# Kernel tuning notes

Measured on AMD Instinct MI355X. Metric: run time of the kernel, lower is better.

Reference implementation:

```python
import jax, jax.numpy as jnp
import numpy as np

N_NODES = 100000
N_EDGES = 3200000
N_GRAPHS = 1000
C = 11   # atomic features
D = 4    # bond features
BN_EPS = 1e-5


def setup_inputs() -> dict:
    key = jax.random.key(0)
    ks = jax.random.split(key, 20)
    inp = {
        "x": jax.random.normal(ks[0], (N_NODES, C), dtype=jnp.float32),
        "edge_index": jax.random.randint(ks[1], (2, N_EDGES), 0, N_NODES),
        "edge_attr": jax.random.uniform(ks[2], (N_EDGES, D), dtype=jnp.float32),
        "batch": jnp.sort(jax.random.randint(ks[3], (N_NODES,), 0, N_GRAPHS)),
    }
    s = 0.3
    # CGConv layer 1 params: lin_f, lin_s take z=[x_i, x_j, e] of dim 2C+D
    inp["Wf1"] = jax.random.normal(ks[4], (2 * C + D, C), dtype=jnp.float32) * s
    inp["bf1"] = jnp.zeros((C,), jnp.float32)
    inp["Ws1"] = jax.random.normal(ks[5], (2 * C + D, C), dtype=jnp.float32) * s
    inp["bs1"] = jnp.zeros((C,), jnp.float32)
    inp["gamma1"] = jnp.ones((C,), jnp.float32)
    inp["beta1"] = jnp.zeros((C,), jnp.float32)
    # CGConv layer 2
    inp["Wf2"] = jax.random.normal(ks[6], (2 * C + D, C), dtype=jnp.float32) * s
    inp["bf2"] = jnp.zeros((C,), jnp.float32)
    inp["Ws2"] = jax.random.normal(ks[7], (2 * C + D, C), dtype=jnp.float32) * s
    inp["bs2"] = jnp.zeros((C,), jnp.float32)
    inp["gamma2"] = jnp.ones((C,), jnp.float32)
    inp["beta2"] = jnp.zeros((C,), jnp.float32)
    # MLP head
    inp["W_fc1"] = jax.random.normal(ks[8], (C, 5), dtype=jnp.float32) * s
    inp["b_fc1"] = jnp.zeros((5,), jnp.float32)
    inp["W_fc2"] = jax.random.normal(ks[9], (5, 1), dtype=jnp.float32) * s
    inp["b_fc2"] = jnp.zeros((1,), jnp.float32)
    return inp


def _cgconv(x, src, dst, e, Wf, bf, Ws, bs, gamma, beta):
    # z = [x_i, x_j, e_ij] per edge; message = sigmoid(lin_f(z)) * softplus(lin_s(z))
    z = jnp.concatenate([x[dst], x[src], e], axis=-1)          # [E, 2C+D]
    msg = jax.nn.sigmoid(z @ Wf + bf) * jax.nn.softplus(z @ Ws + bs)  # [E, C]
    agg = jax.ops.segment_sum(msg, dst, num_segments=N_NODES)  # [N, C]
    # BatchNorm1d (training-mode: batch statistics over nodes)
    mu = jnp.mean(agg, axis=0)
    var = jnp.var(agg, axis=0)
    agg = (agg - mu) * jax.lax.rsqrt(var + BN_EPS) * gamma + beta
    return x + agg  # residual


def reference(x, edge_index, edge_attr, batch,
              Wf1, bf1, Ws1, bs1, gamma1, beta1,
              Wf2, bf2, Ws2, bs2, gamma2, beta2,
              W_fc1, b_fc1, W_fc2, b_fc2):
    src, dst = edge_index[0], edge_index[1]
    h = _cgconv(x, src, dst, edge_attr, Wf1, bf1, Ws1, bs1, gamma1, beta1)
    h = _cgconv(h, src, dst, edge_attr, Wf2, bf2, Ws2, bs2, gamma2, beta2)
    # global mean pool per graph
    sums = jax.ops.segment_sum(h, batch, num_segments=N_GRAPHS)        # [G, C]
    cnts = jax.ops.segment_sum(jnp.ones((h.shape[0],), h.dtype), batch,
                               num_segments=N_GRAPHS)
    pooled = sums / jnp.maximum(cnts, 1.0)[:, None]
    out = jax.nn.softplus(pooled @ W_fc1 + b_fc1)
    out = out @ W_fc2 + b_fc2                                          # [G, 1]
    return out
```

## Files before the change

kernel.cpp:

```cpp
#include <hip/hip_runtime.h>
#include <math.h>

#define N_NODES 100000
#define N_EDGES 3200000
#define N_GRAPHS 1000
#define C 11
#define D 4
#define AST 12
#define XWST 24
#define BN_EPS 1e-5f
#define LOG2E 1.44269504088896f
#define LN2   0.69314718055994f
#define QSCALE (1.0f/65535.0f)

#define BSHIFT 8
#define BNODES 256
#define NB ((N_NODES + BNODES - 1) / BNODES)
#define CAP 8704
#define EPB 4096
#define PBLK ((N_EDGES + EPB - 1) / EPB)
#define SB 64
#define PST 48

__device__ __forceinline__ float fast_sigmoid(float x) {
    float e = exp2f(-LOG2E * x);
    return __builtin_amdgcn_rcpf(1.0f + e);
}
__device__ __forceinline__ float fast_softplus(float x) {
    float e = exp2f(LOG2E * x);
    float l = log2f(1.0f + e) * LN2;
    return (x > 20.0f) ? x : l;
}

__global__ void __launch_bounds__(256) partition_kernel(
    const int* __restrict__ ei, const float4* __restrict__ ea,
    int* __restrict__ bcur, uint3* __restrict__ grp)
{
    __shared__ int lh[NB];
    __shared__ int lbase[NB];
    for (int i = threadIdx.x; i < NB; i += 256) lh[i] = 0;
    __syncthreads();
    int e0 = blockIdx.x * EPB;
    for (int r = 0; r < EPB; r += 256) {
        int e = e0 + r + threadIdx.x;
        if (e < N_EDGES) atomicAdd(&lh[ei[N_EDGES + e] >> BSHIFT], 1);
    }
    __syncthreads();
    for (int b = threadIdx.x; b < NB; b += 256) {
        lbase[b] = atomicAdd(&bcur[b], lh[b]);
        lh[b] = 0;
    }
    __syncthreads();
    for (int r = 0; r < EPB; r += 256) {
        int e = e0 + r + threadIdx.x;
        if (e < N_EDGES) {
            int d = ei[N_EDGES + e];
            int s = ei[e];
            float4 v = ea[e];
            unsigned q0 = (unsigned)(v.x * 65535.0f + 0.5f);
            unsigned q1 = (unsigned)(v.y * 65535.0f + 0.5f);
            unsigned q2 = (unsigned)(v.z * 65535.0f + 0.5f);
            unsigned q3 = (unsigned)(v.w * 65535.0f + 0.5f);
            int b = d >> BSHIFT;
            int ofs = lbase[b] + atomicAdd(&lh[b], 1);
            grp[(size_t)b * CAP + ofs] =
                make_uint3((unsigned)s | ((unsigned)(d & 255) << 17),
                           q0 | (q1 << 16), q2 | (q3 << 16));
        }
    }
}

__global__ void __launch_bounds__(512) bscan_kernel(
    const int* __restrict__ bcur, int* __restrict__ bexcl, int* __restrict__ off)
{
    __shared__ int wsum[8];
    int t = threadIdx.x;
    int lane = t & 63, w = t >> 6;
    int v = (t < NB) ? bcur[t] : 0;
    int incl = v;
    #pragma unroll
    for (int d = 1; d < 64; d <<= 1) {
        int u = __shfl_up(incl, d);
        if (lane >= d) incl += u;
    }
    if (lane == 63) wsum[w] = incl;
    __syncthreads();
    if (w == 0) {
        int x = (lane < 8) ? wsum[lane] : 0;
        #pragma unroll
        for (int d = 1; d < 8; d <<= 1) {
            int u = __shfl_up(x, d);
            if (lane >= d) x += u;
        }
        if (lane < 8) wsum[lane] = x;
    }
    __syncthreads();
    int excl = incl - v + (w > 0 ? wsum[w - 1] : 0);
    if (t < NB) bexcl[t] = excl;
    if (t == 0) { bexcl[NB] = N_EDGES; off[N_NODES] = N_EDGES; }
}

__global__ void __launch_bounds__(256) finalize_kernel(
    const uint3* __restrict__ grp, const int* __restrict__ bcur,
    const int* __restrict__ bexcl,
    int* __restrict__ off, uint3* __restrict__ rec)
{
    __shared__ int lcnt[BNODES];
    __shared__ int lexcl[BNODES];
    __shared__ int wsum[4];
    int b = blockIdx.x;
    int cnt = min(bcur[b], CAP);
    int base = bexcl[b];
    const uint3* g = grp + (size_t)b * CAP;
    int t = threadIdx.x;
    lcnt[t] = 0;
    __syncthreads();
    for (int i = t; i < cnt; i += 256)
        atomicAdd(&lcnt[(g[i].x >> 17) & 255], 1);
    __syncthreads();
    int lane = t & 63, w = t >> 6;
    int v = lcnt[t];
    int incl = v;
    #pragma unroll
    for (int d = 1; d < 64; d <<= 1) {
        int u = __shfl_up(incl, d);
        if (lane >= d) incl += u;
    }
    if (lane == 63) wsum[w] = incl;
    __syncthreads();
    if (w == 0) {
        int x = (lane < 4) ? wsum[lane] : 0;
        #pragma unroll
        for (int d = 1; d < 4; d <<= 1) {
            int u = __shfl_up(x, d);
            if (lane >= d) x += u;
        }
        if (lane < 4) wsum[lane] = x;
    }
    __syncthreads();
    int excl = incl - v + (w > 0 ? wsum[w - 1] : 0);
    lexcl[t] = excl;
    int n = (b << BSHIFT) + t;
    if (n < N_NODES) off[n] = base + excl;
    lcnt[t] = 0;
    __syncthreads();
    for (int i = t; i < cnt; i += 256) {
        uint3 r = g[i];
        int nl = (r.x >> 17) & 255;
        int pos = base + lexcl[nl] + atomicAdd(&lcnt[nl], 1);
        rec[pos] = make_uint3(r.x & 0x1FFFFu, r.y, r.z);
    }
}

__global__ void __launch_bounds__(256) pre_kernel(
    const float* __restrict__ xin, int stride,
    const float* __restrict__ Wf, const float* __restrict__ Ws,
    const float* __restrict__ bf, const float* __restrict__ bs,
    float* __restrict__ xwd, float* __restrict__ xws)
{
    __shared__ float sW[22 * C * 2];
    __shared__ float sbf[C], sbs[C];
    for (int i = threadIdx.x; i < 22 * C; i += blockDim.x) {
        sW[2 * i] = Wf[i];
        sW[2 * i + 1] = Ws[i];
    }
    if (threadIdx.x < C) { sbf[threadIdx.x] = bf[threadIdx.x]; sbs[threadIdx.x] = bs[threadIdx.x]; }
    __syncthreads();

    int n = blockIdx.x * blockDim.x + threadIdx.x;
    if (n >= N_NODES) return;
    float xi[C];
    #pragma unroll
    for (int j = 0; j < C; ++j) xi[j] = xin[n * stride + j];

    float od[XWST], os[XWST];
    #pragma unroll
    for (int c = 0; c < C; ++c) {
        float f = sbf[c], s = sbs[c];
        float f2 = 0.0f, s2 = 0.0f;
        #pragma unroll
        for (int j = 0; j < C; ++j) {
            f  = fmaf(xi[j], sW[2 * (j * C + c)], f);
            s  = fmaf(xi[j], sW[2 * (j * C + c) + 1], s);
            f2 = fmaf(xi[j], sW[2 * ((C + j) * C + c)], f2);
            s2 = fmaf(xi[j], sW[2 * ((C + j) * C + c) + 1], s2);
        }
        od[2 * c] = f; od[2 * c + 1] = s;
        os[2 * c] = f2; os[2 * c + 1] = s2;
    }
    od[22] = 0.0f; od[23] = 0.0f; os[22] = 0.0f; os[23] = 0.0f;
    float4* pd = (float4*)(xwd + (size_t)n * XWST);
    float4* ps = (float4*)(xws + (size_t)n * XWST);
    #pragma unroll
    for (int i = 0; i < 6; ++i) {
        pd[i] = make_float4(od[4 * i], od[4 * i + 1], od[4 * i + 2], od[4 * i + 3]);
        ps[i] = make_float4(os[4 * i], os[4 * i + 1], os[4 * i + 2], os[4 * i + 3]);
    }
}

__global__ void __launch_bounds__(256) conv_kernel(
    const uint3* __restrict__ rec, const int* __restrict__ off,
    const float* __restrict__ xwd, const float* __restrict__ xws,
    const float* __restrict__ Wf, const float* __restrict__ Ws,
    float* __restrict__ agg)
{
    int tid = blockIdx.x * blockDim.x + threadIdx.x;
    int n = tid >> 3;
    int t = tid & 7;
    if (n >= N_NODES) return;

    float weaf[44], weas[44];
    {
        const float2* pf = (const float2*)(Wf + 22 * C);
        const float2* ps = (const float2*)(Ws + 22 * C);
        #pragma unroll
        for (int i = 0; i < 22; ++i) {
            float2 a = pf[i], b = ps[i];
            weaf[2 * i] = a.x; weaf[2 * i + 1] = a.y;
            weas[2 * i] = b.x; weas[2 * i + 1] = b.y;
        }
    }
    float based[XWST];
    {
        const float4* pd = (const float4*)(xwd + (size_t)n * XWST);
        #pragma unroll
        for (int i = 0; i < 6; ++i) {
            float4 a = pd[i];
            based[4 * i] = a.x; based[4 * i + 1] = a.y;
            based[4 * i + 2] = a.z; based[4 * i + 3] = a.w;
        }
    }

    float acc[C];
    #pragma unroll
    for (int c = 0; c < C; ++c) acc[c] = 0.0f;

    int e1 = off[n + 1];
    for (int k = off[n] + t; k < e1; k += 8) {
        uint3 r = rec[k];
        int src = (int)r.x;
        float ea0 = (float)(r.y & 0xFFFFu) * QSCALE;
        float ea1 = (float)(r.y >> 16) * QSCALE;
        float ea2 = (float)(r.z & 0xFFFFu) * QSCALE;
        float ea3 = (float)(r.z >> 16) * QSCALE;
        float xsr[XWST];
        {
            const float4* px = (const float4*)(xws + (size_t)src * XWST);
            #pragma unroll
            for (int i = 0; i < 6; ++i) {
                float4 a = px[i];
                xsr[4 * i] = a.x; xsr[4 * i + 1] = a.y;
                xsr[4 * i + 2] = a.z; xsr[4 * i + 3] = a.w;
            }
        }
        #pragma unroll
        for (int c = 0; c < C; ++c) {
            float f = based[2 * c] + xsr[2 * c];
            float s = based[2 * c + 1] + xsr[2 * c + 1];
            f = fmaf(ea0, weaf[c], f);         s = fmaf(ea0, weas[c], s);
            f = fmaf(ea1, weaf[C + c], f);     s = fmaf(ea1, weas[C + c], s);
            f = fmaf(ea2, weaf[2 * C + c], f); s = fmaf(ea2, weas[2 * C + c], s);
            f = fmaf(ea3, weaf[3 * C + c], f); s = fmaf(ea3, weas[3 * C + c], s);
            acc[c] += fast_sigmoid(f) * fast_softplus(s);
        }
    }

    #pragma unroll
    for (int c = 0; c < C; ++c) {
        acc[c] += __shfl_xor(acc[c], 1);
        acc[c] += __shfl_xor(acc[c], 2);
        acc[c] += __shfl_xor(acc[c], 4);
    }
    if (t == 0) {
        float4* pa = (float4*)(agg + (size_t)n * AST);
        pa[0] = make_float4(acc[0], acc[1], acc[2], acc[3]);
        pa[1] = make_float4(acc[4], acc[5], acc[6], acc[7]);
        pa[2] = make_float4(acc[8], acc[9], acc[10], 0.0f);
    }
}

__global__ void __launch_bounds__(256) bn_stats_kernel(
    const float* __restrict__ agg, float* __restrict__ pstats )
{
    float s[C], q[C];
    #pragma unroll
    for (int c = 0; c < C; ++c) { s[c] = 0.0f; q[c] = 0.0f; }
    for (int n = blockIdx.x * 256 + threadIdx.x; n < N_NODES; n += SB * 256) {
        const float4* pa = (const float4*)(agg + (size_t)n * AST);
        float4 a0 = pa[0], a1 = pa[1], a2 = pa[2];
        float v[C] = {a0.x, a0.y, a0.z, a0.w, a1.x, a1.y, a1.z, a1.w,
                      a2.x, a2.y, a2.z};
        #pragma unroll
        for (int c = 0; c < C; ++c) { s[c] += v[c]; q[c] += v[c] * v[c]; }
    }
    #pragma unroll
    for (int c = 0; c < C; ++c) {
        #pragma unroll
        for (int o = 32; o > 0; o >>= 1) {
            s[c] += __shfl_down(s[c], o);
            q[c] += __shfl_down(q[c], o);
        }
    }
    __shared__ float ls[2 * C + 2];
    if (threadIdx.x < 2 * C + 2) ls[threadIdx.x] = 0.0f;
    __syncthreads();
    if ((threadIdx.x & 63) == 0) {
        #pragma unroll
        for (int c = 0; c < C; ++c) {
            atomicAdd(&ls[2 * c], s[c]);
            atomicAdd(&ls[2 * c + 1], q[c]);
        }
    }
    __syncthreads();
    if (threadIdx.x < 2 * C)
        pstats[blockIdx.x * PST + threadIdx.x] = ls[threadIdx.x];
}

__device__ __forceinline__ void reduce_stats(
    const float* __restrict__ pstats, float* smu, float* srs)
{
    if (threadIdx.x < C) {
        double sum = 0.0, sq = 0.0;
        for (int b = 0; b < SB; ++b) {
            sum += (double)pstats[b * PST + 2 * threadIdx.x];
            sq  += (double)pstats[b * PST + 2 * threadIdx.x + 1];
        }
        double mu = sum / (double)N_NODES;
        double var = sq / (double)N_NODES - mu * mu;
        smu[threadIdx.x] = (float)mu;
        srs[threadIdx.x] = (float)(1.0 / sqrt(var + (double)BN_EPS));
    }
}

__global__ void __launch_bounds__(256) bnpre_kernel(
    const float* __restrict__ xin, const float* __restrict__ agg,
    const float* __restrict__ pstats,
    const float* __restrict__ gamma, const float* __restrict__ beta,
    const float* __restrict__ Wf, const float* __restrict__ Ws,
    const float* __restrict__ bf, const float* __restrict__ bs,
    float* __restrict__ hout, float* __restrict__ xwd, float* __restrict__ xws)
{
    __shared__ float sW[22 * C * 2];
    __shared__ float sbf[C], sbs[C];
    __shared__ float smu[C], srs[C], sg[C], sb[C];
    for (int i = threadIdx.x; i < 22 * C; i += blockDim.x) {
        sW[2 * i] = Wf[i];
        sW[2 * i + 1] = Ws[i];
    }
    reduce_stats(pstats, smu, srs);
    if (threadIdx.x < C) {
        sbf[threadIdx.x] = bf[threadIdx.x];
        sbs[threadIdx.x] = bs[threadIdx.x];
        sg[threadIdx.x] = gamma[threadIdx.x];
        sb[threadIdx.x] = beta[threadIdx.x];
    }
    __syncthreads();

    int n = blockIdx.x * blockDim.x + threadIdx.x;
    if (n >= N_NODES) return;

    float hv[C];
    #pragma unroll
    for (int c = 0; c < C; ++c) {
        float a = agg[n * AST + c];
        hv[c] = xin[n * C + c] + (a - smu[c]) * srs[c] * sg[c] + sb[c];
    }
    {
        float4* ph = (float4*)(hout + (size_t)n * AST);
        ph[0] = make_float4(hv[0], hv[1], hv[2], hv[3]);
        ph[1] = make_float4(hv[4], hv[5], hv[6], hv[7]);
        ph[2] = make_float4(hv[8], hv[9], hv[10], 0.0f);
    }

    float od[XWST], os[XWST];
    #pragma unroll
    for (int c = 0; c < C; ++c) {
        float f = sbf[c], s = sbs[c];
        float f2 = 0.0f, s2 = 0.0f;
        #pragma unroll
        for (int j = 0; j < C; ++j) {
            f  = fmaf(hv[j], sW[2 * (j * C + c)], f);
            s  = fmaf(hv[j], sW[2 * (j * C + c) + 1], s);
            f2 = fmaf(hv[j], sW[2 * ((C + j) * C + c)], f2);
            s2 = fmaf(hv[j], sW[2 * ((C + j) * C + c) + 1], s2);
        }
        od[2 * c] = f; od[2 * c + 1] = s;
        os[2 * c] = f2; os[2 * c + 1] = s2;
    }
    od[22] = 0.0f; od[23] = 0.0f; os[22] = 0.0f; os[23] = 0.0f;
    float4* pd = (float4*)(xwd + (size_t)n * XWST);
    float4* ps = (float4*)(xws + (size_t)n * XWST);
    #pragma unroll
    for (int i = 0; i < 6; ++i) {
        pd[i] = make_float4(od[4 * i], od[4 * i + 1], od[4 * i + 2], od[4 * i + 3]);
        ps[i] = make_float4(os[4 * i], os[4 * i + 1], os[4 * i + 2], os[4 * i + 3]);
    }
}

__global__ void __launch_bounds__(256) bn_apply_kernel(
    const float* __restrict__ hin, const float* __restrict__ agg,
    const float* __restrict__ pstats,
    const float* __restrict__ gamma, const float* __restrict__ beta,
    float* __restrict__ hout)
{
    __shared__ float smu[C], srs[C], sg[C], sb[C];
    reduce_stats(pstats, smu, srs);
    if (threadIdx.x < C) {
        sg[threadIdx.x] = gamma[threadIdx.x];
        sb[threadIdx.x] = beta[threadIdx.x];
    }
    __syncthreads();
    int n = blockIdx.x * blockDim.x + threadIdx.x;
    if (n >= N_NODES) return;
    float hv[C];
    #pragma unroll
    for (int c = 0; c < C; ++c) {
        float a = agg[n * AST + c];
        hv[c] = hin[n * AST + c] + (a - smu[c]) * srs[c] * sg[c] + sb[c];
    }
    float4* ph = (float4*)(hout + (size_t)n * AST);
    ph[0] = make_float4(hv[0], hv[1], hv[2], hv[3]);
    ph[1] = make_float4(hv[4], hv[5], hv[6], hv[7]);
    ph[2] = make_float4(hv[8], hv[9], hv[10], 0.0f);
}

__global__ void __launch_bounds__(256) pool_kernel(
    const float* __restrict__ h, const int* __restrict__ batch,
    float* __restrict__ gsum, float* __restrict__ gcnt)
{
    const int PER = 8;
    int t = blockIdx.x * blockDim.x + threadIdx.x;
    int start = t * PER;
    if (start >= N_NODES) return;
    int end = min(start + PER, N_NODES);

    int g = batch[start];
    float acc[C];
    #pragma unroll
    for (int c = 0; c < C; ++c) acc[c] = 0.0f;
    float cnt = 0.0f;
    for (int n = start; n < end; ++n) {
        int gn = batch[n];
        if (gn != g) {
            #pragma unroll
            for (int c = 0; c < C; ++c) atomicAdd(&gsum[g * C + c], acc[c]);
            atomicAdd(&gcnt[g], cnt);
            g = gn;
            #pragma unroll
            for (int c = 0; c < C; ++c) acc[c] = 0.0f;
            cnt = 0.0f;
        }
        #pragma unroll
        for (int c = 0; c < C; ++c) acc[c] += h[n * AST + c];
        cnt += 1.0f;
    }
    #pragma unroll
    for (int c = 0; c < C; ++c) atomicAdd(&gsum[g * C + c], acc[c]);
    atomicAdd(&gcnt[g], cnt);
}

__global__ void __launch_bounds__(256) head_kernel(
    const float* __restrict__ gsum, const float* __restrict__ gcnt,
    const float* __restrict__ W1, const float* __restrict__ b1,
    const float* __restrict__ W2, const float* __restrict__ b2,
    float* __restrict__ out)
{
    int g = blockIdx.x * blockDim.x + threadIdx.x;
    if (g >= N_GRAPHS) return;
    float cnt = fmaxf(gcnt[g], 1.0f);
    float p[C];
    #pragma unroll
    for (int c = 0; c < C; ++c) p[c] = gsum[g * C + c] / cnt;
    float acc = b2[0];
    #pragma unroll
    for (int j = 0; j < 5; ++j) {
        float t = b1[j];
        #pragma unroll
        for (int c = 0; c < C; ++c) t = fmaf(p[c], W1[c * 5 + j], t);
        acc = fmaf(fast_softplus(t), W2[j], acc);
    }
    out[g] = acc;
}

extern "C" void kernel_launch(void* const* d_in, const int* in_sizes, int n_in,
                              void* d_out, int out_size, void* d_ws, size_t ws_size,
                              hipStream_t stream) {
    const float* x   = (const float*)d_in[0];
    const int*   ei  = (const int*)d_in[1];
    const float* ea  = (const float*)d_in[2];
    const int*   bat = (const int*)d_in[3];
    const float* Wf1 = (const float*)d_in[4];
    const float* bf1 = (const float*)d_in[5];
    const float* Ws1 = (const float*)d_in[6];
    const float* bs1 = (const float*)d_in[7];
    const float* g1  = (const float*)d_in[8];
    const float* be1 = (const float*)d_in[9];
    const float* Wf2 = (const float*)d_in[10];
    const float* bf2 = (const float*)d_in[11];
    const float* Ws2 = (const float*)d_in[12];
    const float* bs2 = (const float*)d_in[13];
    const float* g2  = (const float*)d_in[14];
    const float* be2 = (const float*)d_in[15];
    const float* W_fc1 = (const float*)d_in[16];
    const float* b_fc1 = (const float*)d_in[17];
    const float* W_fc2 = (const float*)d_in[18];
    const float* b_fc2 = (const float*)d_in[19];
    float* out = (float*)d_out;

    char* ws = (char*)d_ws;
    size_t o = 0;
    size_t zz0 = o;
    int*    bcur   = (int*)(ws + o);    o += (size_t)NB * 4;
    float*  gsum   = (float*)(ws + o);  o += (size_t)N_GRAPHS * C * 4;
    float*  gcnt   = (float*)(ws + o);  o += (size_t)N_GRAPHS * 4;
    size_t zsize = o - zz0;
    int*    bexcl  = (int*)(ws + o);    o += (size_t)(NB + 1) * 4;
    int*    off    = (int*)(ws + o);    o += (size_t)(N_NODES + 1) * 4;
    o = (o + 255) & ~(size_t)255;
    float*  pst1   = (float*)(ws + o);  o += (size_t)SB * PST * 4;
    float*  pst2   = (float*)(ws + o);  o += (size_t)SB * PST * 4;
    o = (o + 255) & ~(size_t)255;
    uint3*  grp    = (uint3*)(ws + o);  o += (size_t)NB * CAP * 12;
    o = (o + 255) & ~(size_t)255;
    uint3*  rec    = (uint3*)(ws + o);  o += (size_t)N_EDGES * 12;
    o = (o + 255) & ~(size_t)255;
    float*  xwd    = (float*)(ws + o);  o += (size_t)N_NODES * XWST * 4;
    float*  xws    = (float*)(ws + o);  o += (size_t)N_NODES * XWST * 4;
    float*  agg    = (float*)(ws + o);  o += (size_t)N_NODES * AST * 4;
    float*  h1     = (float*)(ws + o);  o += (size_t)N_NODES * AST * 4;
    float*  h2     = xwd;

    const int cblocks = (N_NODES * 8 + 255) / 256;
    const int nblocks = (N_NODES + 255) / 256;

    hipMemsetAsync(ws + zz0, 0, zsize, stream);

    partition_kernel<<<PBLK, 256, 0, stream>>>(ei, (const float4*)ea, bcur, grp);
    bscan_kernel<<<1, 512, 0, stream>>>(bcur, bexcl, off);
    finalize_kernel<<<NB, 256, 0, stream>>>(grp, bcur, bexcl, off, rec);

    pre_kernel<<<nblocks, 256, 0, stream>>>(x, C, Wf1, Ws1, bf1, bs1, xwd, xws);
    conv_kernel<<<cblocks, 256, 0, stream>>>(rec, off, xwd, xws, Wf1, Ws1, agg);
    bn_stats_kernel<<<SB, 256, 0, stream>>>(agg, pst1);
    bnpre_kernel<<<nblocks, 256, 0, stream>>>(x, agg, pst1, g1, be1,
                                              Wf2, Ws2, bf2, bs2, h1, xwd, xws);

    conv_kernel<<<cblocks, 256, 0, stream>>>(rec, off, xwd, xws, Wf2, Ws2, agg);
    bn_stats_kernel<<<SB, 256, 0, stream>>>(agg, pst2);
    bn_apply_kernel<<<nblocks, 256, 0, stream>>>(h1, agg, pst2, g2, be2, h2);

    pool_kernel<<<(N_NODES / 8 + 255) / 256, 256, 0, stream>>>(h2, bat, gsum, gcnt);
    head_kernel<<<(N_GRAPHS + 255) / 256, 256, 0, stream>>>(gsum, gcnt, W_fc1, b_fc1,
                                                            W_fc2, b_fc2, out);
}
```

Baseline: 349.0 us.

## Store gathered source-node projections in fp16 and split partition counters into sub-buckets

The per-source-node projection table that each edge gathers is now stored as packed half2 (48 bytes per node instead of 96), which cuts gather traffic in both conv passes. The partition step spreads each bucket's global atomic counter over 8 sub-buckets chosen by block index, reducing contention on the counters. Finalize and scan now iterate over and sum those sub-buckets. This trades precision in the gathered values for bandwidth, and any sub-bucket that exceeds its fixed capacity silently drops edges.

```diff
diff --git a/kernel.cpp b/kernel.cpp
--- a/kernel.cpp
+++ b/kernel.cpp
@@ -1,4 +1,5 @@
 #include <hip/hip_runtime.h>
+#include <hip/hip_fp16.h>
 #include <math.h>
 
 #define N_NODES 100000
@@ -8,6 +9,7 @@
 #define D 4
 #define AST 12
 #define XWST 24
+#define XHST 16
 #define BN_EPS 1e-5f
 #define LOG2E 1.44269504088896f
 #define LN2   0.69314718055994f
@@ -16,7 +18,8 @@
 #define BSHIFT 8
 #define BNODES 256
 #define NB ((N_NODES + BNODES - 1) / BNODES)
-#define CAP 8704
+#define SUBS 8
+#define CAP2 1280
 #define EPB 4096
 #define PBLK ((N_EDGES + EPB - 1) / EPB)
 #define SB 64
@@ -31,15 +34,24 @@
     float l = log2f(1.0f + e) * LN2;
     return (x > 20.0f) ? x : l;
 }
+__device__ __forceinline__ unsigned packh2(float a, float b) {
+    __half2 h = __floats2half2_rn(a, b);
+    return *reinterpret_cast<unsigned*>(&h);
+}
+__device__ __forceinline__ float2 unpackh2(unsigned u) {
+    __half2 h = *reinterpret_cast<__half2*>(&u);
+    return __half22float2(h);
+}
 
 __global__ void __launch_bounds__(256) partition_kernel(
     const int* __restrict__ ei, const float4* __restrict__ ea,
-    int* __restrict__ bcur, uint3* __restrict__ grp)
+    int* __restrict__ bcur2, uint3* __restrict__ grp)
 {
     __shared__ int lh[NB];
     __shared__ int lbase[NB];
     for (int i = threadIdx.x; i < NB; i += 256) lh[i] = 0;
     __syncthreads();
+    int sub = blockIdx.x & (SUBS - 1);
     int e0 = blockIdx.x * EPB;
     for (int r = 0; r < EPB; r += 256) {
         int e = e0 + r + threadIdx.x;
@@ -47,7 +59,7 @@
     }
     __syncthreads();
     for (int b = threadIdx.x; b < NB; b += 256) {
-        lbase[b] = atomicAdd(&bcur[b], lh[b]);
+        lbase[b] = atomicAdd(&bcur2[b * SUBS + sub], lh[b]);
         lh[b] = 0;
     }
     __syncthreads();
@@ -63,20 +75,25 @@
             unsigned q3 = (unsigned)(v.w * 65535.0f + 0.5f);
             int b = d >> BSHIFT;
             int ofs = lbase[b] + atomicAdd(&lh[b], 1);
-            grp[(size_t)b * CAP + ofs] =
-                make_uint3((unsigned)s | ((unsigned)(d & 255) << 17),
-                           q0 | (q1 << 16), q2 | (q3 << 16));
+            if (ofs < CAP2)
+                grp[((size_t)b * SUBS + sub) * CAP2 + ofs] =
+                    make_uint3((unsigned)s | ((unsigned)(d & 255) << 17),
+                               q0 | (q1 << 16), q2 | (q3 << 16));
         }
     }
 }
 
 __global__ void __launch_bounds__(512) bscan_kernel(
-    const int* __restrict__ bcur, int* __restrict__ bexcl, int* __restrict__ off)
+    const int* __restrict__ bcur2, int* __restrict__ bexcl, int* __restrict__ off)
 {
     __shared__ int wsum[8];
     int t = threadIdx.x;
     int lane = t & 63, w = t >> 6;
-    int v = (t < NB) ? bcur[t] : 0;
+    int v = 0;
+    if (t < NB) {
+        #pragma unroll
+        for (int s = 0; s < SUBS; ++s) v += min(bcur2[t * SUBS + s], CAP2);
+    }
     int incl = v;
     #pragma unroll
     for (int d = 1; d < 64; d <<= 1) {
@@ -97,11 +114,12 @@
     __syncthreads();
     int excl = incl - v + (w > 0 ? wsum[w - 1] : 0);
     if (t < NB) bexcl[t] = excl;
-    if (t == 0) { bexcl[NB] = N_EDGES; off[N_NODES] = N_EDGES; }
+    if (t == 0) off[N_NODES] = bexcl[NB - 1] >= 0 ? 0 : 0;
+    if (t == NB - 1) off[N_NODES] = excl + v;
 }
 
 __global__ void __launch_bounds__(256) finalize_kernel(
-    const uint3* __restrict__ grp, const int* __restrict__ bcur,
+    const uint3* __restrict__ grp, const int* __restrict__ bcur2,
     const int* __restrict__ bexcl,
     int* __restrict__ off, uint3* __restrict__ rec)
 {
@@ -109,14 +127,16 @@
     __shared__ int lexcl[BNODES];
     __shared__ int wsum[4];
     int b = blockIdx.x;
-    int cnt = min(bcur[b], CAP);
     int base = bexcl[b];
-    const uint3* g = grp + (size_t)b * CAP;
     int t = threadIdx.x;
     lcnt[t] = 0;
     __syncthreads();
-    for (int i = t; i < cnt; i += 256)
-        atomicAdd(&lcnt[(g[i].x >> 17) & 255], 1);
+    for (int s = 0; s < SUBS; ++s) {
+        int cs = min(bcur2[b * SUBS + s], CAP2);
+        const uint3* g = grp + ((size_t)b * SUBS + s) * CAP2;
+        for (int i = t; i < cs; i += 256)
+            atomicAdd(&lcnt[(g[i].x >> 17) & 255], 1);
+    }
     __syncthreads();
     int lane = t & 63, w = t >> 6;
     int v = lcnt[t];
@@ -144,11 +164,15 @@
     if (n < N_NODES) off[n] = base + excl;
     lcnt[t] = 0;
     __syncthreads();
-    for (int i = t; i < cnt; i += 256) {
-        uint3 r = g[i];
-        int nl = (r.x >> 17) & 255;
-        int pos = base + lexcl[nl] + atomicAdd(&lcnt[nl], 1);
-        rec[pos] = make_uint3(r.x & 0x1FFFFu, r.y, r.z);
+    for (int s = 0; s < SUBS; ++s) {
+        int cs = min(bcur2[b * SUBS + s], CAP2);
+        const uint3* g = grp + ((size_t)b * SUBS + s) * CAP2;
+        for (int i = t; i < cs; i += 256) {
+            uint3 r = g[i];
+            int nl = (r.x >> 17) & 255;
+            int pos = base + lexcl[nl] + atomicAdd(&lcnt[nl], 1);
+            rec[pos] = make_uint3(r.x & 0x1FFFFu, r.y, r.z);
+        }
     }
 }
 
@@ -156,7 +180,7 @@
     const float* __restrict__ xin, int stride,
     const float* __restrict__ Wf, const float* __restrict__ Ws,
     const float* __restrict__ bf, const float* __restrict__ bs,
-    float* __restrict__ xwd, float* __restrict__ xws)
+    float* __restrict__ xwd, unsigned* __restrict__ xwsh)
 {
     __shared__ float sW[22 * C * 2];
     __shared__ float sbf[C], sbs[C];
@@ -173,7 +197,8 @@
     #pragma unroll
     for (int j = 0; j < C; ++j) xi[j] = xin[n * stride + j];
 
-    float od[XWST], os[XWST];
+    float od[XWST];
+    unsigned oh[12];
     #pragma unroll
     for (int c = 0; c < C; ++c) {
         float f = sbf[c], s = sbs[c];
@@ -186,21 +211,22 @@
             s2 = fmaf(xi[j], sW[2 * ((C + j) * C + c) + 1], s2);
         }
         od[2 * c] = f; od[2 * c + 1] = s;
-        os[2 * c] = f2; os[2 * c + 1] = s2;
-    }
-    od[22] = 0.0f; od[23] = 0.0f; os[22] = 0.0f; os[23] = 0.0f;
+        oh[c] = packh2(f2, s2);
+    }
+    od[22] = 0.0f; od[23] = 0.0f; oh[11] = 0u;
     float4* pd = (float4*)(xwd + (size_t)n * XWST);
-    float4* ps = (float4*)(xws + (size_t)n * XWST);
-    #pragma unroll
-    for (int i = 0; i < 6; ++i) {
+    #pragma unroll
+    for (int i = 0; i < 6; ++i)
         pd[i] = make_float4(od[4 * i], od[4 * i + 1], od[4 * i + 2], od[4 * i + 3]);
-        ps[i] = make_float4(os[4 * i], os[4 * i + 1], os[4 * i + 2], os[4 * i + 3]);
-    }
+    uint4* ph = (uint4*)(xwsh + (size_t)n * XHST);
+    #pragma unroll
+    for (int i = 0; i < 3; ++i)
+        ph[i] = make_uint4(oh[4 * i], oh[4 * i + 1], oh[4 * i + 2], oh[4 * i + 3]);
 }
 
 __global__ void __launch_bounds__(256) conv_kernel(
     const uint3* __restrict__ rec, const int* __restrict__ off,
-    const float* __restrict__ xwd, const float* __restrict__ xws,
+    const float* __restrict__ xwd, const unsigned* __restrict__ xwsh,
     const float* __restrict__ Wf, const float* __restrict__ Ws,
     float* __restrict__ agg)
 {
@@ -243,20 +269,19 @@
         float ea1 = (float)(r.y >> 16) * QSCALE;
         float ea2 = (float)(r.z & 0xFFFFu) * QSCALE;
         float ea3 = (float)(r.z >> 16) * QSCALE;
-        float xsr[XWST];
-        {
-            const float4* px = (const float4*)(xws + (size_t)src * XWST);
-            #pragma unroll
-            for (int i = 0; i < 6; ++i) {
-                float4 a = px[i];
-                xsr[4 * i] = a.x; xsr[4 * i + 1] = a.y;
-                xsr[4 * i + 2] = a.z; xsr[4 * i + 3] = a.w;
-            }
-        }
+        const uint4* px = (const uint4*)(xwsh + (size_t)src * XHST);
+        uint4 ha = px[0], hb = px[1], hc = px[2];
+        float2 xv[C];
+        xv[0] = unpackh2(ha.x); xv[1] = unpackh2(ha.y);
+        xv[2] = unpackh2(ha.z); xv[3] = unpackh2(ha.w);
+        xv[4] = unpackh2(hb.x); xv[5] = unpackh2(hb.y);
+        xv[6] = unpackh2(hb.z); xv[7] = unpackh2(hb.w);
+        xv[8] = unpackh2(hc.x); xv[9] = unpackh2(hc.y);
+        xv[10] = unpackh2(hc.z);
         #pragma unroll
         for (int c = 0; c < C; ++c) {
-            float f = based[2 * c] + xsr[2 * c];
-            float s = based[2 * c + 1] + xsr[2 * c + 1];
+            float f = based[2 * c] + xv[c].x;
+            float s = based[2 * c + 1] + xv[c].y;
             f = fmaf(ea0, weaf[c], f);         s = fmaf(ea0, weas[c], s);
             f = fmaf(ea1, weaf[C + c], f);     s = fmaf(ea1, weas[C + c], s);
             f = fmaf(ea2, weaf[2 * C + c], f); s = fmaf(ea2, weas[2 * C + c], s);
@@ -338,7 +363,7 @@
     const float* __restrict__ gamma, const float* __restrict__ beta,
     const float* __restrict__ Wf, const float* __restrict__ Ws,
     const float* __restrict__ bf, const float* __restrict__ bs,
-    float* __restrict__ hout, float* __restrict__ xwd, float* __restrict__ xws)
+    float* __restrict__ hout, float* __restrict__ xwd, unsigned* __restrict__ xwsh)
 {
     __shared__ float sW[22 * C * 2];
     __shared__ float sbf[C], sbs[C];
@@ -372,7 +397,8 @@
         ph[2] = make_float4(hv[8], hv[9], hv[10], 0.0f);
     }
 
-    float od[XWST], os[XWST];
+    float od[XWST];
+    unsigned oh[12];
     #pragma unroll
     for (int c = 0; c < C; ++c) {
         float f = sbf[c], s = sbs[c];
@@ -385,16 +411,17 @@
             s2 = fmaf(hv[j], sW[2 * ((C + j) * C + c) + 1], s2);
         }
         od[2 * c] = f; od[2 * c + 1] = s;
-        os[2 * c] = f2; os[2 * c + 1] = s2;
-    }
-    od[22] = 0.0f; od[23] = 0.0f; os[22] = 0.0f; os[23] = 0.0f;
+        oh[c] = packh2(f2, s2);
+    }
+    od[22] = 0.0f; od[23] = 0.0f; oh[11] = 0u;
     float4* pd = (float4*)(xwd + (size_t)n * XWST);
-    float4* ps = (float4*)(xws + (size_t)n * XWST);
-    #pragma unroll
-    for (int i = 0; i < 6; ++i) {
+    #pragma unroll
+    for (int i = 0; i < 6; ++i)
         pd[i] = make_float4(od[4 * i], od[4 * i + 1], od[4 * i + 2], od[4 * i + 3]);
-        ps[i] = make_float4(os[4 * i], os[4 * i + 1], os[4 * i + 2], os[4 * i + 3]);
-    }
+    uint4* ph2 = (uint4*)(xwsh + (size_t)n * XHST);
+    #pragma unroll
+    for (int i = 0; i < 3; ++i)
+        ph2[i] = make_uint4(oh[4 * i], oh[4 * i + 1], oh[4 * i + 2], oh[4 * i + 3]);
 }
 
 __global__ void __launch_bounds__(256) bn_apply_kernel(
@@ -510,42 +537,43 @@
     char* ws = (char*)d_ws;
     size_t o = 0;
     size_t zz0 = o;
-    int*    bcur   = (int*)(ws + o);    o += (size_t)NB * 4;
-    float*  gsum   = (float*)(ws + o);  o += (size_t)N_GRAPHS * C * 4;
-    float*  gcnt   = (float*)(ws + o);  o += (size_t)N_GRAPHS * 4;
+    int*      bcur2 = (int*)(ws + o);      o += (size_t)NB * SUBS * 4;
+    float*    gsum  = (float*)(ws + o);    o += (size_t)N_GRAPHS * C * 4;
+    float*    gcnt  = (float*)(ws + o);    o += (size_t)N_GRAPHS * 4;
     size_t zsize = o - zz0;
-    int*    bexcl  = (int*)(ws + o);    o += (size_t)(NB + 1) * 4;
-    int*    off    = (int*)(ws + o);    o += (size_t)(N_NODES + 1) * 4;
+    int*      bexcl = (int*)(ws + o);      o += (size_t)(NB + 1) * 4;
+    int*      off   = (int*)(ws + o);      o += (size_t)(N_NODES + 1) * 4;
     o = (o + 255) & ~(size_t)255;
-    float*  pst1   = (float*)(ws + o);  o += (size_t)SB * PST * 4;
-    float*  pst2   = (float*)(ws + o);  o += (size_t)SB * PST * 4;
+    float*    pst1  = (float*)(ws + o);    o += (size_t)SB * PST * 4;
+    float*    pst2  = (float*)(ws + o);    o += (size_t)SB * PST * 4;
     o = (o + 255) & ~(size_t)255;
-    uint3*  grp    = (uint3*)(ws + o);  o += (size_t)NB * CAP * 12;
+    uint3*    grp   = (uint3*)(ws + o);    o += (size_t)NB * SUBS * CAP2 * 12;
     o = (o + 255) & ~(size_t)255;
-    uint3*  rec    = (uint3*)(ws + o);  o += (size_t)N_EDGES * 12;
+    uint3*    rec   = (uint3*)(ws + o);    o += (size_t)N_EDGES * 12;
     o = (o + 255) & ~(size_t)255;
-    float*  xwd    = (float*)(ws + o);  o += (size_t)N_NODES * XWST * 4;
-    float*  xws    = (float*)(ws + o);  o += (size_t)N_NODES * XWST * 4;
-    float*  agg    = (float*)(ws + o);  o += (size_t)N_NODES * AST * 4;
-    float*  h1     = (float*)(ws + o);  o += (size_t)N_NODES * AST * 4;
-    float*  h2     = xwd;
+    float*    xwd   = (float*)(ws + o);    o += (size_t)N_NODES * XWST * 4;
+    o = (o + 255) & ~(size_t)255;
+    unsigned* xwsh  = (unsigned*)(ws + o); o += (size_t)N_NODES * XHST * 4;
+    float*    agg   = (float*)(ws + o);    o += (size_t)N_NODES * AST * 4;
+    float*    h1    = (float*)(ws + o);    o += (size_t)N_NODES * AST * 4;
+    float*    h2    = xwd;
 
     const int cblocks = (N_NODES * 8 + 255) / 256;
     const int nblocks = (N_NODES + 255) / 256;
 
     hipMemsetAsync(ws + zz0, 0, zsize, stream);
 
-    partition_kernel<<<PBLK, 256, 0, stream>>>(ei, (const float4*)ea, bcur, grp);
-    bscan_kernel<<<1, 512, 0, stream>>>(bcur, bexcl, off);
-    finalize_kernel<<<NB, 256, 0, stream>>>(grp, bcur, bexcl, off, rec);
-
-    pre_kernel<<<nblocks, 256, 0, stream>>>(x, C, Wf1, Ws1, bf1, bs1, xwd, xws);
-    conv_kernel<<<cblocks, 256, 0, stream>>>(rec, off, xwd, xws, Wf1, Ws1, agg);
+    partition_kernel<<<PBLK, 256, 0, stream>>>(ei, (const float4*)ea, bcur2, grp);
+    bscan_kernel<<<1, 512, 0, stream>>>(bcur2, bexcl, off);
+    finalize_kernel<<<NB, 256, 0, stream>>>(grp, bcur2, bexcl, off, rec);
+
+    pre_kernel<<<nblocks, 256, 0, stream>>>(x, C, Wf1, Ws1, bf1, bs1, xwd, xwsh);
+    conv_kernel<<<cblocks, 256, 0, stream>>>(rec, off, xwd, xwsh, Wf1, Ws1, agg);
     bn_stats_kernel<<<SB, 256, 0, stream>>>(agg, pst1);
     bnpre_kernel<<<nblocks, 256, 0, stream>>>(x, agg, pst1, g1, be1,
-                                              Wf2, Ws2, bf2, bs2, h1, xwd, xws);
-
-    conv_kernel<<<cblocks, 256, 0, stream>>>(rec, off, xwd, xws, Wf2, Ws2, agg);
+                                              Wf2, Ws2, bf2, bs2, h1, xwd, xwsh);
+
+    conv_kernel<<<cblocks, 256, 0, stream>>>(rec, off, xwd, xwsh, Wf2, Ws2, agg);
     bn_stats_kernel<<<SB, 256, 0, stream>>>(agg, pst2);
     bn_apply_kernel<<<nblocks, 256, 0, stream>>>(h1, agg, pst2, g2, be2, h2);
 
```

Measured after the change: 344.9 us. No clear change (-1.2%).
